# Optimization experiments

Hardware: AMD Instinct MI355X
Metric: run time of the kernel (lower is better)

The kernel has to match this reference:

```python
import jax, jax.numpy as jnp
import numpy as np
import math

B, S, D = 4, 4096, 2048
HEAD_DIM = 128  # dim_model // head_nums = 2048 // 16
DEPTH = 12


def setup_inputs() -> dict:
    key = jax.random.key(0)
    ks = jax.random.split(key, 8)
    std = 0.1
    return {
        "x": jax.random.normal(ks[0], (B, S, D), dtype=jnp.float32),
        "WQ": jax.random.normal(ks[1], (D, 2 * HEAD_DIM), dtype=jnp.float32) * (D ** -0.5),
        "WK": jax.random.normal(ks[2], (D, 2 * HEAD_DIM), dtype=jnp.float32) * (D ** -0.5),
        "WV": jax.random.normal(ks[3], (D, 2 * HEAD_DIM), dtype=jnp.float32) * (D ** -0.5),
        "lambda_q1": jax.random.normal(ks[4], (HEAD_DIM,), dtype=jnp.float32) * std,
        "lambda_q2": jax.random.normal(ks[5], (HEAD_DIM,), dtype=jnp.float32) * std,
        "lambda_k1": jax.random.normal(ks[6], (HEAD_DIM,), dtype=jnp.float32) * std,
        "lambda_k2": jax.random.normal(ks[7], (HEAD_DIM,), dtype=jnp.float32) * std,
    }


def reference(x, WQ, WK, WV, lambda_q1, lambda_q2, lambda_k1, lambda_k2):
    scale = HEAD_DIM ** -0.5
    lambda_init = 0.8 - 0.6 * math.exp(-0.3 * DEPTH)

    q = x @ WQ                      # [B, S, 2*hd]
    k = x @ WK
    v = x @ WV                      # [B, S, 2*hd]
    q1, q2 = q[..., :HEAD_DIM], q[..., HEAD_DIM:]
    k1, k2 = k[..., :HEAD_DIM], k[..., HEAD_DIM:]

    a1 = jnp.einsum("bqd,bkd->bqk", q1, k1) * scale  # [B, S, S]
    a2 = jnp.einsum("bqd,bkd->bqk", q2, k2) * scale

    lambda_1 = jnp.exp(jnp.sum(lambda_q1 * lambda_k1))
    lambda_2 = jnp.exp(jnp.sum(lambda_q2 * lambda_k2))
    lam = lambda_1 + lambda_2 + lambda_init

    attn = jax.nn.softmax(a1, axis=-1) - lam * jax.nn.softmax(a2, axis=-1)
    return jnp.einsum("bqk,bkd->bqd", attn, v)  # [B, S, 2*hd]
```

## Files before the change

### kernel.cpp

```cpp
#include <hip/hip_runtime.h>
#include <stdint.h>

typedef unsigned short u16;
typedef __attribute__((ext_vector_type(4))) float f32x4;
typedef __attribute__((ext_vector_type(16))) float f32x16;
typedef __attribute__((ext_vector_type(8))) short s16x8;
typedef __attribute__((ext_vector_type(8))) __bf16 bf16x8;
typedef __attribute__((ext_vector_type(8))) unsigned short u16x8;
typedef __attribute__((ext_vector_type(4))) unsigned short u16x4;
typedef __attribute__((ext_vector_type(4))) uint32_t u32x4;
typedef __attribute__((ext_vector_type(2))) uint32_t u32x2;

__device__ __forceinline__ f32x4 mfma16(s16x8 a, s16x8 b, f32x4 c) {
  return __builtin_amdgcn_mfma_f32_16x16x32_bf16(
      __builtin_bit_cast(bf16x8, a), __builtin_bit_cast(bf16x8, b), c, 0, 0, 0);
}
__device__ __forceinline__ f32x16 mfma32(s16x8 a, s16x8 b, f32x16 c) {
  return __builtin_amdgcn_mfma_f32_32x32x16_bf16(
      __builtin_bit_cast(bf16x8, a), __builtin_bit_cast(bf16x8, b), c, 0, 0, 0);
}

__device__ __forceinline__ void gl_lds16(const u16* g, u16* l) {
  __builtin_amdgcn_global_load_lds(
      (const __attribute__((address_space(1))) void*)g,
      (__attribute__((address_space(3))) void*)l, 16, 0, 0);
}

__device__ __forceinline__ u16 bf16rne(float f) {
  uint32_t u = __builtin_bit_cast(uint32_t, f);
  u += 0x7fffu + ((u >> 16) & 1u);
  return (u16)(u >> 16);
}

__global__ void pre_kernel(const float* __restrict__ x, const float* __restrict__ WQ,
                           const float* __restrict__ WK, const float* __restrict__ WV,
                           const float* __restrict__ lq1, const float* __restrict__ lq2,
                           const float* __restrict__ lk1, const float* __restrict__ lk2,
                           u16* __restrict__ xb, u16* __restrict__ Wt,
                           float* __restrict__ lamp, float qscale) {
  const int blk = blockIdx.x, tid = threadIdx.x;
  if (blk < 16384) {
    size_t i = ((size_t)blk * 256 + tid) * 8;
    f32x4 a = *(const f32x4*)(x + i);
    f32x4 b = *(const f32x4*)(x + i + 4);
    u16x8 o;
#pragma unroll
    for (int j = 0; j < 4; ++j) { o[j] = bf16rne(a[j]); o[4 + j] = bf16rne(b[j]); }
    *(u16x8*)(xb + i) = o;
  } else if (blk < 22528) {
    int i = (blk - 16384) * 256 + tid;
    int r = i >> 11, k = i & 2047;
    int sel = r >> 8, c = r & 255;
    const float* W = (sel == 0) ? WQ : (sel == 1) ? WK : WV;
    float v = W[(size_t)k * 256 + c];
    if (sel == 0) v *= qscale;
    Wt[i] = bf16rne(v);
  } else {
    if (tid < 64) {
      int t = tid;
      float d1 = lq1[t] * lk1[t] + lq1[t + 64] * lk1[t + 64];
      float d2 = lq2[t] * lk2[t] + lq2[t + 64] * lk2[t + 64];
#pragma unroll
      for (int off = 32; off; off >>= 1) {
        d1 += __shfl_xor(d1, off);
        d2 += __shfl_xor(d2, off);
      }
      if (t == 0) *lamp = expf(d1) + expf(d2) + (0.8f - 0.6f * expf(-3.6f));
    }
  }
}

__global__ __launch_bounds__(256) void proj_gemm(const u16* __restrict__ xb, const u16* __restrict__ Wt,
                                                 u16* __restrict__ Qb, u16* __restrict__ Kb,
                                                 u16* __restrict__ Vt) {
  const int bid = blockIdx.x;
  const int xcd = bid & 7, j = bid >> 3;
  const int m0 = (xcd * 16 + (j / 6)) * 128;
  const int n0 = (j % 6) * 128;
  const int tid = threadIdx.x, lane = tid & 63, w = tid >> 6;
  const int ln = lane & 15, quad = lane >> 4;
  const int wm = w & 1, wn = w >> 1;
  __shared__ __align__(16) u16 As[2][128 * 32];
  __shared__ __align__(16) u16 Bs[2][128 * 32];
  f32x4 acc[4][4];
#pragma unroll
  for (int i = 0; i < 4; ++i)
#pragma unroll
    for (int jj = 0; jj < 4; ++jj) acc[i][jj] = f32x4{0.f, 0.f, 0.f, 0.f};

  auto stage = [&](int kk, int bi) {
#pragma unroll
    for (int i = 0; i < 2; ++i) {
      int p = tid + i * 256;
      int row = p >> 2, cg = (p & 3) ^ (row & 3);
      gl_lds16(xb + (size_t)(m0 + row) * 2048 + kk + cg * 8, As[bi] + (size_t)(p - lane) * 8);
      gl_lds16(Wt + (size_t)(n0 + row) * 2048 + kk + cg * 8, Bs[bi] + (size_t)(p - lane) * 8);
    }
  };

  stage(0, 0);
  for (int t = 0; t < 64; ++t) {
    __syncthreads();
    if (t + 1 < 64) stage((t + 1) * 32, (t + 1) & 1);
    const u16* Asb = As[t & 1];
    const u16* Bsb = Bs[t & 1];
    s16x8 a[4];
#pragma unroll
    for (int mt = 0; mt < 4; ++mt) {
      int r = wm * 64 + mt * 16 + ln;
      a[mt] = *(const s16x8*)(Asb + r * 32 + ((quad ^ (r & 3)) * 8));
    }
#pragma unroll
    for (int nt = 0; nt < 4; ++nt) {
      int r = wn * 64 + nt * 16 + ln;
      s16x8 bf = *(const s16x8*)(Bsb + r * 32 + ((quad ^ (r & 3)) * 8));
#pragma unroll
      for (int mt = 0; mt < 4; ++mt) acc[mt][nt] = mfma16(a[mt], bf, acc[mt][nt]);
    }
  }
#pragma unroll
  for (int mt = 0; mt < 4; ++mt)
#pragma unroll
    for (int nt = 0; nt < 4; ++nt) {
      int row0 = m0 + wm * 64 + mt * 16 + quad * 4;
      int col = n0 + wn * 64 + nt * 16 + ln;
      int sel = col >> 8, c = col & 255;
      u16x4 vv;
#pragma unroll
      for (int jj = 0; jj < 4; ++jj) vv[jj] = bf16rne(acc[mt][nt][jj]);
      if (sel == 2) {
        int b = row0 >> 12, s = row0 & 4095;
        *(u16x4*)(Vt + (size_t)b * 1048576 + (size_t)c * 4096 + s) = vv;
      } else {
        u16* dst = (sel == 0) ? Qb : Kb;
#pragma unroll
        for (int jj = 0; jj < 4; ++jj) dst[(size_t)(row0 + jj) * 256 + c] = vv[jj];
      }
    }
}

__global__ __launch_bounds__(512, 2) void attn_kernel(const u16* __restrict__ Qb,
                                                      const u16* __restrict__ Kb,
                                                      const u16* __restrict__ Vt,
                                                      const float* __restrict__ lamp,
                                                      float* __restrict__ out) {
  const int bid = blockIdx.x;
  const int xcd = bid & 7;
  const int b = xcd >> 1;
  const int qt = ((bid >> 3) << 1) + (xcd & 1);
  const int tid = threadIdx.x, lane = tid & 63, w = tid >> 6;
  const int l5 = lane & 31, lh = lane >> 5;
  const int m = w & 1, kt = (w >> 1) & 1, qh = w >> 2;

  __shared__ __align__(16) char smem[134144];
  float* buf0 = (float*)smem;
  float* buf1 = (float*)(smem + 66560);
  float* ls = (float*)(smem + 133120);

  const u16* Kg0 = Kb + ((size_t)b * 4096) * 256;
  const u16* Vg0 = Vt + (size_t)b * 1048576;

  auto stage = [&](int kb, char* base) {
    u16* Ks = (u16*)base;
    u16* Vs = (u16*)(base + 32768);
#pragma unroll
    for (int i = 0; i < 4; ++i) {
      int p = tid + i * 512;
      int row = p >> 5, c = p & 31;
      int cg = (c & 16) | ((c ^ row) & 15);
      gl_lds16(Kg0 + (size_t)(kb + row) * 256 + cg * 8, Ks + (size_t)(p - lane) * 8);
    }
#pragma unroll
    for (int i = 0; i < 4; ++i) {
      int p = tid + i * 512;
      int row = p >> 3, c = p & 7;
      int cg = c ^ (row & 7);
      gl_lds16(Vg0 + (size_t)row * 4096 + kb + cg * 8, Vs + (size_t)(p - lane) * 8);
    }
  };

  stage(0, smem);

  s16x8 bq[8];
  {
    const u16* qp =
        Qb + ((size_t)(b * 4096 + qt * 64 + qh * 32 + l5)) * 256 + m * 128 + lh * 8;
#pragma unroll
    for (int s = 0; s < 8; ++s) bq[s] = *(const s16x8*)(qp + s * 16);
  }

  f32x16 O[8];
#pragma unroll
  for (int ct = 0; ct < 8; ++ct)
#pragma unroll
    for (int r = 0; r < 16; ++r) O[ct][r] = 0.f;
  float l_run = 0.f;

  for (int t = 0; t < 64; ++t) {
    __syncthreads();
    if (t + 1 < 64) stage((t + 1) * 64, smem + ((t + 1) & 1) * 65536);

    char* base = smem + (t & 1) * 65536;
    u16* Ks = (u16*)base;
    u16* Vs = (u16*)(base + 32768);

    f32x16 Sa, Sb;
#pragma unroll
    for (int r = 0; r < 16; ++r) { Sa[r] = 0.f; Sb[r] = 0.f; }
#pragma unroll
    for (int s = 0; s < 8; s += 2) {
      int row = kt * 32 + l5;
      int c0 = m * 16 + s * 2 + lh;
      int c1 = m * 16 + (s + 1) * 2 + lh;
      s16x8 a0 = *(const s16x8*)(Ks + row * 256 + (((c0 & 16) | ((c0 ^ row) & 15))) * 8);
      s16x8 a1 = *(const s16x8*)(Ks + row * 256 + (((c1 & 16) | ((c1 ^ row) & 15))) * 8);
      Sa = mfma32(a0, bq[s], Sa);
      Sb = mfma32(a1, bq[s + 1], Sb);
    }

    s16x8 vfr0[8], vfr1[8];
#pragma unroll
    for (int ct = 0; ct < 8; ++ct) {
      int row = ct * 32 + l5;
      int c0v = (kt * 32) / 8 + lh;
      int c1v = (kt * 32 + 16) / 8 + lh;
      vfr0[ct] = *(const s16x8*)(Vs + row * 64 + ((c0v ^ (row & 7)) * 8));
      vfr1[ct] = *(const s16x8*)(Vs + row * 64 + ((c1v ^ (row & 7)) * 8));
    }

    uint32_t P[8];
#pragma unroll
    for (int d = 0; d < 8; ++d) {
      float p0 = __builtin_amdgcn_exp2f(Sa[2 * d] + Sb[2 * d]);
      float p1 = __builtin_amdgcn_exp2f(Sa[2 * d + 1] + Sb[2 * d + 1]);
      l_run += p0 + p1;
      P[d] = (uint32_t)bf16rne(p0) | ((uint32_t)bf16rne(p1) << 16);
    }

#pragma unroll
    for (int ks = 0; ks < 2; ++ks) {
      u32x2 s02 = __builtin_amdgcn_permlane32_swap(P[ks * 4 + 0], P[ks * 4 + 2], false, false);
      u32x2 s13 = __builtin_amdgcn_permlane32_swap(P[ks * 4 + 1], P[ks * 4 + 3], false, false);
      u32x4 fd;
      fd[0] = s02[0]; fd[1] = s13[0]; fd[2] = s02[1]; fd[3] = s13[1];
      s16x8 pf = __builtin_bit_cast(s16x8, fd);
      if (ks == 0) {
#pragma unroll
        for (int ct = 0; ct < 8; ++ct) O[ct] = mfma32(vfr0[ct], pf, O[ct]);
      } else {
#pragma unroll
        for (int ct = 0; ct < 8; ++ct) O[ct] = mfma32(vfr1[ct], pf, O[ct]);
      }
    }
  }

  float lam = *lamp;
  l_run += __shfl_xor(l_run, 32);
  __syncthreads();
  if (lane < 32) ls[w * 32 + l5] = l_run;
  float* bufm = m ? buf1 : buf0;
  const int qb0 = qh * 32;
  if (kt == 1) {
#pragma unroll
    for (int ct = 0; ct < 8; ++ct)
#pragma unroll
      for (int r = 0; r < 16; ++r) {
        int vcol = ct * 32 + (r & 3) + 8 * (r >> 2) + 4 * lh;
        bufm[vcol * 65 + qb0 + l5] = O[ct][r];
      }
  }
  __syncthreads();
  if (kt == 0) {
    float linv = 1.f / (ls[w * 32 + l5] + ls[(w | 2) * 32 + l5]);
#pragma unroll
    for (int ct = 0; ct < 8; ++ct)
#pragma unroll
      for (int r = 0; r < 16; ++r) {
        int vcol = ct * 32 + (r & 3) + 8 * (r >> 2) + 4 * lh;
        bufm[vcol * 65 + qb0 + l5] = (O[ct][r] + bufm[vcol * 65 + qb0 + l5]) * linv;
      }
  }
  __syncthreads();
  float* og = out + ((size_t)(b * 4096 + qt * 64)) * 256;
  const int col = tid & 255, half = tid >> 8;
#pragma unroll
  for (int j2 = 0; j2 < 32; ++j2) {
    int q = half * 32 + j2;
    float v = buf0[col * 65 + q] - lam * buf1[col * 65 + q];
    og[(size_t)q * 256 + col] = v;
  }
}

extern "C" void kernel_launch(void* const* d_in, const int* in_sizes, int n_in,
                              void* d_out, int out_size, void* d_ws, size_t ws_size,
                              hipStream_t stream) {
  (void)in_sizes; (void)n_in; (void)out_size; (void)ws_size;
  const float* x   = (const float*)d_in[0];
  const float* WQ  = (const float*)d_in[1];
  const float* WK  = (const float*)d_in[2];
  const float* WV  = (const float*)d_in[3];
  const float* lq1 = (const float*)d_in[4];
  const float* lq2 = (const float*)d_in[5];
  const float* lk1 = (const float*)d_in[6];
  const float* lk2 = (const float*)d_in[7];
  float* out = (float*)d_out;

  char* ws = (char*)d_ws;
  u16* xb = (u16*)ws;   ws += (size_t)16384 * 2048 * 2;
  u16* Wt = (u16*)ws;   ws += (size_t)768 * 2048 * 2;
  u16* Qb = (u16*)ws;   ws += (size_t)16384 * 256 * 2;
  u16* Kb = (u16*)ws;   ws += (size_t)16384 * 256 * 2;
  u16* Vt = (u16*)ws;   ws += (size_t)16384 * 256 * 2;
  float* lamp = (float*)ws;

  const float qscale = 0.0883883476f * 1.44269504f;

  hipLaunchKernelGGL(pre_kernel, dim3(22529), dim3(256), 0, stream,
                     x, WQ, WK, WV, lq1, lq2, lk1, lk2, xb, Wt, lamp, qscale);
  hipLaunchKernelGGL(proj_gemm, dim3(768), dim3(256), 0, stream, xb, Wt, Qb, Kb, Vt);
  hipLaunchKernelGGL(attn_kernel, dim3(256), dim3(512), 0, stream, Qb, Kb, Vt, lamp, out);
}
```

Measured before the change: 384.2 us.

## Fuse fp32-to-bf16 conversion of x into the projection GEMM

The projection GEMM now stages fp32 `x` tiles straight into LDS with an XOR swizzle over 8 column groups. It converts them to bf16 in registers just before the MFMA, so the separate pass that wrote a bf16 copy of `x` is gone. That removes a full read and write of the large activation tensor plus the intermediate buffer. The query scale moves from the pre-scaled weights into the GEMM epilogue, which slightly changes rounding order. In exchange, the GEMM reads twice the bytes per A tile for each N-tile pass, uses more LDS, and does extra VALU conversion work in the inner loop.

```diff
diff --git a/kernel.cpp b/kernel.cpp
--- a/kernel.cpp
+++ b/kernel.cpp
@@ -32,47 +32,34 @@
   return (u16)(u >> 16);
 }
 
-__global__ void pre_kernel(const float* __restrict__ x, const float* __restrict__ WQ,
-                           const float* __restrict__ WK, const float* __restrict__ WV,
+__global__ void pre_kernel(const float* __restrict__ WQ, const float* __restrict__ WK,
+                           const float* __restrict__ WV,
                            const float* __restrict__ lq1, const float* __restrict__ lq2,
                            const float* __restrict__ lk1, const float* __restrict__ lk2,
-                           u16* __restrict__ xb, u16* __restrict__ Wt,
-                           float* __restrict__ lamp, float qscale) {
+                           u16* __restrict__ Wt, float* __restrict__ lamp) {
   const int blk = blockIdx.x, tid = threadIdx.x;
-  if (blk < 16384) {
-    size_t i = ((size_t)blk * 256 + tid) * 8;
-    f32x4 a = *(const f32x4*)(x + i);
-    f32x4 b = *(const f32x4*)(x + i + 4);
-    u16x8 o;
-#pragma unroll
-    for (int j = 0; j < 4; ++j) { o[j] = bf16rne(a[j]); o[4 + j] = bf16rne(b[j]); }
-    *(u16x8*)(xb + i) = o;
-  } else if (blk < 22528) {
-    int i = (blk - 16384) * 256 + tid;
+  if (blk < 6144) {
+    int i = blk * 256 + tid;
     int r = i >> 11, k = i & 2047;
     int sel = r >> 8, c = r & 255;
     const float* W = (sel == 0) ? WQ : (sel == 1) ? WK : WV;
-    float v = W[(size_t)k * 256 + c];
-    if (sel == 0) v *= qscale;
-    Wt[i] = bf16rne(v);
-  } else {
-    if (tid < 64) {
-      int t = tid;
-      float d1 = lq1[t] * lk1[t] + lq1[t + 64] * lk1[t + 64];
-      float d2 = lq2[t] * lk2[t] + lq2[t + 64] * lk2[t + 64];
-#pragma unroll
-      for (int off = 32; off; off >>= 1) {
-        d1 += __shfl_xor(d1, off);
-        d2 += __shfl_xor(d2, off);
-      }
-      if (t == 0) *lamp = expf(d1) + expf(d2) + (0.8f - 0.6f * expf(-3.6f));
-    }
-  }
-}
-
-__global__ __launch_bounds__(256) void proj_gemm(const u16* __restrict__ xb, const u16* __restrict__ Wt,
+    Wt[i] = bf16rne(W[(size_t)k * 256 + c]);
+  } else if (tid < 64) {
+    int t = tid;
+    float d1 = lq1[t] * lk1[t] + lq1[t + 64] * lk1[t + 64];
+    float d2 = lq2[t] * lk2[t] + lq2[t + 64] * lk2[t + 64];
+#pragma unroll
+    for (int off = 32; off; off >>= 1) {
+      d1 += __shfl_xor(d1, off);
+      d2 += __shfl_xor(d2, off);
+    }
+    if (t == 0) *lamp = expf(d1) + expf(d2) + (0.8f - 0.6f * expf(-3.6f));
+  }
+}
+
+__global__ __launch_bounds__(256) void proj_gemm(const float* __restrict__ x, const u16* __restrict__ Wt,
                                                  u16* __restrict__ Qb, u16* __restrict__ Kb,
-                                                 u16* __restrict__ Vt) {
+                                                 u16* __restrict__ Vt, float qscale) {
   const int bid = blockIdx.x;
   const int xcd = bid & 7, j = bid >> 3;
   const int m0 = (xcd * 16 + (j / 6)) * 128;
@@ -80,7 +67,7 @@
   const int tid = threadIdx.x, lane = tid & 63, w = tid >> 6;
   const int ln = lane & 15, quad = lane >> 4;
   const int wm = w & 1, wn = w >> 1;
-  __shared__ __align__(16) u16 As[2][128 * 32];
+  __shared__ __align__(16) float Af[2][128 * 32];
   __shared__ __align__(16) u16 Bs[2][128 * 32];
   f32x4 acc[4][4];
 #pragma unroll
@@ -89,11 +76,18 @@
     for (int jj = 0; jj < 4; ++jj) acc[i][jj] = f32x4{0.f, 0.f, 0.f, 0.f};
 
   auto stage = [&](int kk, int bi) {
+#pragma unroll
+    for (int i = 0; i < 4; ++i) {
+      int p = tid + i * 256;
+      int row = p >> 3, c = p & 7;
+      int cg = c ^ (row & 7);
+      gl_lds16((const u16*)(x + (size_t)(m0 + row) * 2048 + kk + cg * 4),
+               (u16*)(Af[bi] + (size_t)(p - lane) * 4));
+    }
 #pragma unroll
     for (int i = 0; i < 2; ++i) {
       int p = tid + i * 256;
       int row = p >> 2, cg = (p & 3) ^ (row & 3);
-      gl_lds16(xb + (size_t)(m0 + row) * 2048 + kk + cg * 8, As[bi] + (size_t)(p - lane) * 8);
       gl_lds16(Wt + (size_t)(n0 + row) * 2048 + kk + cg * 8, Bs[bi] + (size_t)(p - lane) * 8);
     }
   };
@@ -102,13 +96,22 @@
   for (int t = 0; t < 64; ++t) {
     __syncthreads();
     if (t + 1 < 64) stage((t + 1) * 32, (t + 1) & 1);
-    const u16* Asb = As[t & 1];
+    const float* Afb = Af[t & 1];
     const u16* Bsb = Bs[t & 1];
     s16x8 a[4];
 #pragma unroll
     for (int mt = 0; mt < 4; ++mt) {
       int r = wm * 64 + mt * 16 + ln;
-      a[mt] = *(const s16x8*)(Asb + r * 32 + ((quad ^ (r & 3)) * 8));
+      int e = r & 7;
+      f32x4 lo = *(const f32x4*)(Afb + r * 32 + (((2 * quad) ^ e) * 4));
+      f32x4 hi = *(const f32x4*)(Afb + r * 32 + (((2 * quad + 1) ^ e) * 4));
+      u16x8 o;
+#pragma unroll
+      for (int jj = 0; jj < 4; ++jj) {
+        o[jj] = __builtin_bit_cast(u16, (__bf16)lo[jj]);
+        o[4 + jj] = __builtin_bit_cast(u16, (__bf16)hi[jj]);
+      }
+      a[mt] = __builtin_bit_cast(s16x8, o);
     }
 #pragma unroll
     for (int nt = 0; nt < 4; ++nt) {
@@ -125,9 +128,10 @@
       int row0 = m0 + wm * 64 + mt * 16 + quad * 4;
       int col = n0 + wn * 64 + nt * 16 + ln;
       int sel = col >> 8, c = col & 255;
+      float sc = (sel == 0) ? qscale : 1.f;
       u16x4 vv;
 #pragma unroll
-      for (int jj = 0; jj < 4; ++jj) vv[jj] = bf16rne(acc[mt][nt][jj]);
+      for (int jj = 0; jj < 4; ++jj) vv[jj] = bf16rne(acc[mt][nt][jj] * sc);
       if (sel == 2) {
         int b = row0 >> 12, s = row0 & 4095;
         *(u16x4*)(Vt + (size_t)b * 1048576 + (size_t)c * 4096 + s) = vv;
@@ -306,7 +310,6 @@
   float* out = (float*)d_out;
 
   char* ws = (char*)d_ws;
-  u16* xb = (u16*)ws;   ws += (size_t)16384 * 2048 * 2;
   u16* Wt = (u16*)ws;   ws += (size_t)768 * 2048 * 2;
   u16* Qb = (u16*)ws;   ws += (size_t)16384 * 256 * 2;
   u16* Kb = (u16*)ws;   ws += (size_t)16384 * 256 * 2;
@@ -315,8 +318,8 @@
 
   const float qscale = 0.0883883476f * 1.44269504f;
 
-  hipLaunchKernelGGL(pre_kernel, dim3(22529), dim3(256), 0, stream,
-                     x, WQ, WK, WV, lq1, lq2, lk1, lk2, xb, Wt, lamp, qscale);
-  hipLaunchKernelGGL(proj_gemm, dim3(768), dim3(256), 0, stream, xb, Wt, Qb, Kb, Vt);
+  hipLaunchKernelGGL(pre_kernel, dim3(6145), dim3(256), 0, stream,
+                     WQ, WK, WV, lq1, lq2, lk1, lk2, Wt, lamp);
+  hipLaunchKernelGGL(proj_gemm, dim3(768), dim3(256), 0, stream, x, Wt, Qb, Kb, Vt, qscale);
   hipLaunchKernelGGL(attn_kernel, dim3(256), dim3(512), 0, stream, Qb, Kb, Vt, lamp, out);
 }
```

Result: slower. 415.5 us (+8.1%).
